# Performance work log

Measured on AMD Instinct MI355X. Metric: run time of the kernel, lower is better.

The kernel has to match this reference:

```python
import jax, jax.numpy as jnp
import numpy as np

N_NODES = 200000
N_GRAPHS = 64
K_SLOTS = 16
LATENT = 128
HID = 128  # hidden_dim // 2


def setup_inputs() -> dict:
    key = jax.random.key(0)
    ks = jax.random.split(key, 8)
    z = jax.random.normal(ks[0], (N_GRAPHS, K_SLOTS, LATENT), dtype=jnp.float32)
    s = jax.random.uniform(ks[1], (N_NODES, K_SLOTS), dtype=jnp.float32)
    batch = jnp.sort(jax.random.randint(ks[2], (N_NODES,), 0, N_GRAPHS))
    sc1 = 1.0 / np.sqrt(LATENT)
    sc2 = 1.0 / np.sqrt(HID)
    W1 = jax.random.normal(ks[3], (LATENT, HID), dtype=jnp.float32) * sc1
    b1 = jnp.zeros((HID,), dtype=jnp.float32)
    W2 = jax.random.normal(ks[4], (HID, HID), dtype=jnp.float32) * sc2
    b2 = jnp.zeros((HID,), dtype=jnp.float32)
    Wp = jax.random.normal(ks[5], (HID, 2), dtype=jnp.float32) * sc2
    bp = jnp.zeros((2,), dtype=jnp.float32)
    Wv = jax.random.normal(ks[6], (HID, 2), dtype=jnp.float32) * sc2
    bv = jnp.zeros((2,), dtype=jnp.float32)
    return {"z": z, "s": s, "batch": batch, "W1": W1, "b1": b1,
            "W2": W2, "b2": b2, "Wp": Wp, "bp": bp, "Wv": Wv, "bv": bv}


def reference(z, s, batch, W1, b1, W2, b2, Wp, bp, Wv, bv):
    # gather per-node latent set: [N, K, D]
    z_expanded = z[batch]
    # weighted sum over K slots -> [N, D]
    node_feat = jnp.einsum('nk,nkd->nd', s, z_expanded)
    # shared MLP: Linear-ReLU-Linear-ReLU
    h = jax.nn.relu(node_feat @ W1 + b1)
    h = jax.nn.relu(h @ W2 + b2)
    # heads
    pos_recon = jnp.tanh(h @ Wp + bp)
    vel_recon = h @ Wv + bv
    return jnp.concatenate([pos_recon, vel_recon], axis=-1)
```

## Files before the change

kernel.cpp:

```cpp
#include <hip/hip_runtime.h>

typedef _Float16 half4 __attribute__((ext_vector_type(4)));
typedef _Float16 half8 __attribute__((ext_vector_type(8)));
typedef float    f32x4 __attribute__((ext_vector_type(4)));

#define MFMA16(a,b,c) __builtin_amdgcn_mfma_f32_16x16x16f16((a),(b),(c),0,0,0)

static constexpr int N_NODES  = 200000;
static constexpr int N_GRAPHS = 64;
static constexpr int SGPG     = 128;
static constexpr int TOTAL_SG = N_GRAPHS * SGPG;

static constexpr size_t WS_ZWT    = 0;
static constexpr size_t WS_W2T    = 262144;
static constexpr size_t WS_WHT    = 294912;
static constexpr size_t WS_GSTART = 299008;


__global__ __launch_bounds__(256) void gnn_prep(
    const int* __restrict__ batch,
    const float* __restrict__ z,
    const float* __restrict__ W1,
    const float* __restrict__ W2,
    const float* __restrict__ Wp,
    const float* __restrict__ Wv,
    int* __restrict__ gstart,
    _Float16* __restrict__ zwt,
    _Float16* __restrict__ w2t,
    _Float16* __restrict__ wht)
{
    const int b = blockIdx.x, t = threadIdx.x;
    if (b < 782) {
        const int i = b * 256 + t;
        if (i < N_NODES) {
            const int bi   = batch[i];
            const int prev = (i == 0) ? -1 : batch[i - 1];
            if (bi != prev)
                for (int g = prev + 1; g <= bi; ++g) gstart[g] = i;
            if (i == N_NODES - 1)
                for (int g = bi + 1; g <= N_GRAPHS; ++g) gstart[g] = N_NODES;
        }
    } else if (b < 846) {
        const int e = (b - 782) * 256 + t;
        const int n = e >> 7, kk = e & 127;
        w2t[e] = (_Float16)W2[kk * 128 + n];
    } else if (b < 854) {
        const int e = (b - 846) * 256 + t;
        const int j = e >> 7, d = e & 127;
        float v = 0.f;
        if (j < 2)      v = Wp[d * 2 + j];
        else if (j < 4) v = Wv[d * 2 + (j - 2)];
        wht[e] = (_Float16)v;
    } else {
        const int p = (b - 854) * 2 + (t >> 7);
        const int g = p >> 4, k = p & 15, d = t & 127;
        const float* zr = z + (g * 16 + k) * 128;
        float a0 = 0.f, a1 = 0.f, a2 = 0.f, a3 = 0.f;
#pragma unroll 8
        for (int c = 0; c < 128; c += 4) {
            a0 += zr[c    ] * W1[(c    ) * 128 + d];
            a1 += zr[c + 1] * W1[(c + 1) * 128 + d];
            a2 += zr[c + 2] * W1[(c + 2) * 128 + d];
            a3 += zr[c + 3] * W1[(c + 3) * 128 + d];
        }
        zwt[(g * 128 + d) * 16 + k] = (_Float16)((a0 + a1) + (a2 + a3));
    }
}

__device__ inline float fast_tanh(float x) {
    x = fminf(fmaxf(x, -15.f), 15.f);
    const float e = __expf(2.f * x);
    return (e - 1.f) / (e + 1.f);
}

__global__ __launch_bounds__(256, 4) void gnn_main(
    const float* __restrict__ s,
    const float* __restrict__ b1,
    const float* __restrict__ b2,
    const float* __restrict__ bp,
    const float* __restrict__ bv,
    const _Float16* __restrict__ zwt,
    const _Float16* __restrict__ w2t,
    const _Float16* __restrict__ wht,
    const int* __restrict__ gstart,
    float* __restrict__ out)
{
    __shared__ char lds[37888];
    half8* a2l = (half8*)lds;
    half4* a3l = (half4*)(lds + 32768);
    float* b1l = (float*)(lds + 36864);
    float* b2l = (float*)(lds + 37376);

    const int tid  = threadIdx.x;
    const int lane = tid & 63;
    const int n16  = lane & 15;
    const int quad = lane >> 4;

#pragma unroll
    for (int r = 0; r < 8; ++r) {
        const int e  = r * 256 + tid;
        const int mo = e >> 8, tp = (e >> 6) & 3, ll = e & 63;
        const int nn = ll & 15, qq = ll >> 4;
        const _Float16* srcp = w2t + (mo * 16 + nn) * 128 + tp * 32 + qq * 4;
        half8 v;
        *(half4*)&v     = *(const half4*)srcp;
        *((half4*)&v+1) = *(const half4*)(srcp + 16);
        a2l[e] = v;
    }
    {
        const int e = tid;
#pragma unroll
        for (int r = 0; r < 2; ++r) {
            const int ee = r * 256 + e;
            const int tt = ee >> 6, ll = ee & 63;
            const int nn = ll & 15, qq = ll >> 4;
            a3l[ee] = *(const half4*)(wht + nn * 128 + tt * 16 + qq * 4);
        }
        if (tid < 128)      b1l[tid] = b1[tid];
        else                b2l[tid - 128] = b2[tid - 128];
    }
    __syncthreads();

    const float bp0 = bp[0], bp1 = bp[1], bv0 = bv[0], bv1 = bv[1];
    f32x4 c3init = {0.f, 0.f, 0.f, 0.f};
    if (quad == 0) { c3init[0] = bp0; c3init[1] = bp1; c3init[2] = bv0; c3init[3] = bv1; }

    const int wid = blockIdx.x * 4 + (tid >> 6);
    const int nw  = gridDim.x * 4;

    for (int sgi = wid; sgi < TOTAL_SG; sgi += nw) {
        const int g    = sgi >> 7;
        const int idx  = sgi & 127;
        const int gs   = gstart[g];
        const int ge   = gstart[g + 1];
        const int base = gs + idx * 32;
        if (base >= ge) continue;

        const int nodeA = base + n16;
        const int nodeB = base + 16 + n16;
        const bool vA = nodeA < ge;
        const bool vB = nodeB < ge;

        half4 bsA = {(_Float16)0.f, (_Float16)0.f, (_Float16)0.f, (_Float16)0.f};
        half4 bsB = bsA;
        if (vA) {
            const f32x4 sv = *(const f32x4*)(s + nodeA * 16 + quad * 4);
            bsA[0] = (_Float16)sv[0]; bsA[1] = (_Float16)sv[1];
            bsA[2] = (_Float16)sv[2]; bsA[3] = (_Float16)sv[3];
        }
        if (vB) {
            const f32x4 sv = *(const f32x4*)(s + nodeB * 16 + quad * 4);
            bsB[0] = (_Float16)sv[0]; bsB[1] = (_Float16)sv[1];
            bsB[2] = (_Float16)sv[2]; bsB[3] = (_Float16)sv[3];
        }

        const _Float16* zg = zwt + g * 2048;
        half4 h1a[8], h1b[8];
#pragma unroll
        for (int mt = 0; mt < 8; ++mt) {
            const half4 a1 = *(const half4*)(zg + (mt * 16 + n16) * 16 + quad * 4);
            const f32x4 cb = *(const f32x4*)(b1l + mt * 16 + quad * 4);
            const f32x4 accA = MFMA16(a1, bsA, cb);
            const f32x4 accB = MFMA16(a1, bsB, cb);
#pragma unroll
            for (int i = 0; i < 4; ++i) {
                h1a[mt][i] = (_Float16)fmaxf(accA[i], 0.f);
                h1b[mt][i] = (_Float16)fmaxf(accB[i], 0.f);
            }
        }

        f32x4 acc3a = c3init, acc3b = c3init;
#pragma unroll
        for (int mo = 0; mo < 8; ++mo) {
            const f32x4 cb = *(const f32x4*)(b2l + mo * 16 + quad * 4);
            f32x4 a2a = cb, a2b = cb;
#pragma unroll
            for (int tp = 0; tp < 4; ++tp) {
                const half8 w = a2l[(mo * 4 + tp) * 64 + lane];
                const half4 wlo = {w[0], w[1], w[2], w[3]};
                const half4 whi = {w[4], w[5], w[6], w[7]};
                a2a = MFMA16(wlo, h1a[tp * 2], a2a);
                a2a = MFMA16(whi, h1a[tp * 2 + 1], a2a);
                a2b = MFMA16(wlo, h1b[tp * 2], a2b);
                a2b = MFMA16(whi, h1b[tp * 2 + 1], a2b);
            }
            half4 h2a, h2b;
#pragma unroll
            for (int i = 0; i < 4; ++i) {
                h2a[i] = (_Float16)fmaxf(a2a[i], 0.f);
                h2b[i] = (_Float16)fmaxf(a2b[i], 0.f);
            }
            const half4 w3 = a3l[mo * 64 + lane];
            acc3a = MFMA16(w3, h2a, acc3a);
            acc3b = MFMA16(w3, h2b, acc3b);
        }

        if (quad == 0) {
            if (vA) {
                f32x4 o;
                o[0] = fast_tanh(acc3a[0]); o[1] = fast_tanh(acc3a[1]);
                o[2] = acc3a[2];            o[3] = acc3a[3];
                *(f32x4*)(out + nodeA * 4) = o;
            }
            if (vB) {
                f32x4 o;
                o[0] = fast_tanh(acc3b[0]); o[1] = fast_tanh(acc3b[1]);
                o[2] = acc3b[2];            o[3] = acc3b[3];
                *(f32x4*)(out + nodeB * 4) = o;
            }
        }
    }
}

extern "C" void kernel_launch(void* const* d_in, const int* in_sizes, int n_in,
                              void* d_out, int out_size, void* d_ws, size_t ws_size,
                              hipStream_t stream)
{
    const float* z     = (const float*)d_in[0];
    const float* s     = (const float*)d_in[1];
    const int*   batch = (const int*)d_in[2];
    const float* W1    = (const float*)d_in[3];
    const float* b1    = (const float*)d_in[4];
    const float* W2    = (const float*)d_in[5];
    const float* b2    = (const float*)d_in[6];
    const float* Wp    = (const float*)d_in[7];
    const float* bp    = (const float*)d_in[8];
    const float* Wv    = (const float*)d_in[9];
    const float* bv    = (const float*)d_in[10];
    float* out = (float*)d_out;

    char* w = (char*)d_ws;
    _Float16* zwt = (_Float16*)(w + WS_ZWT);
    _Float16* w2t = (_Float16*)(w + WS_W2T);
    _Float16* wht = (_Float16*)(w + WS_WHT);
    int* gstart   = (int*)(w + WS_GSTART);

    hipLaunchKernelGGL(gnn_prep, dim3(1366), dim3(256), 0, stream,
                       batch, z, W1, W2, Wp, Wv, gstart, zwt, w2t, wht);
    hipLaunchKernelGGL(gnn_main, dim3(1024), dim3(256), 0, stream,
                       s, b1, b2, bp, bv, zwt, w2t, wht, gstart, out);
}
```

Baseline: 113.7 us.

## Process fixed 64-node windows per wave, handling graph boundaries with masked MFMAs

Drops the gstart boundary computation from the prep kernel. The main kernel now walks contiguous 64-node windows, reads batch directly, and uses masked per-graph MFMA accumulation when a window spans several graphs. Each wave now handles four 16-node tiles instead of two, so every W2 fragment read from LDS is reused across more MFMAs, and conversions use packed cvt_pkrtz. The cost is higher register pressure, which is why launch bounds drop to 3 waves per SIMD and the grid shrinks. The window indexing assumes N_NODES is a multiple of 64.

```diff
diff --git a/kernel.cpp b/kernel.cpp
--- a/kernel.cpp
+++ b/kernel.cpp
@@ -1,5 +1,7 @@
 #include <hip/hip_runtime.h>
 
+typedef _Float16 half2 __attribute__((ext_vector_type(2)));
+typedef __fp16   fp16x2 __attribute__((ext_vector_type(2)));
 typedef _Float16 half4 __attribute__((ext_vector_type(4)));
 typedef _Float16 half8 __attribute__((ext_vector_type(8)));
 typedef float    f32x4 __attribute__((ext_vector_type(4)));
@@ -7,52 +9,37 @@
 #define MFMA16(a,b,c) __builtin_amdgcn_mfma_f32_16x16x16f16((a),(b),(c),0,0,0)
 
 static constexpr int N_NODES  = 200000;
-static constexpr int N_GRAPHS = 64;
-static constexpr int SGPG     = 128;
-static constexpr int TOTAL_SG = N_GRAPHS * SGPG;
-
-static constexpr size_t WS_ZWT    = 0;
-static constexpr size_t WS_W2T    = 262144;
-static constexpr size_t WS_WHT    = 294912;
-static constexpr size_t WS_GSTART = 299008;
+static constexpr int N_WIN    = N_NODES / 64;
+
+static constexpr size_t WS_ZWT = 0;
+static constexpr size_t WS_W2T = 262144;
+static constexpr size_t WS_WHT = 294912;
 
 
 __global__ __launch_bounds__(256) void gnn_prep(
-    const int* __restrict__ batch,
     const float* __restrict__ z,
     const float* __restrict__ W1,
     const float* __restrict__ W2,
     const float* __restrict__ Wp,
     const float* __restrict__ Wv,
-    int* __restrict__ gstart,
     _Float16* __restrict__ zwt,
     _Float16* __restrict__ w2t,
     _Float16* __restrict__ wht)
 {
     const int b = blockIdx.x, t = threadIdx.x;
-    if (b < 782) {
-        const int i = b * 256 + t;
-        if (i < N_NODES) {
-            const int bi   = batch[i];
-            const int prev = (i == 0) ? -1 : batch[i - 1];
-            if (bi != prev)
-                for (int g = prev + 1; g <= bi; ++g) gstart[g] = i;
-            if (i == N_NODES - 1)
-                for (int g = bi + 1; g <= N_GRAPHS; ++g) gstart[g] = N_NODES;
-        }
-    } else if (b < 846) {
-        const int e = (b - 782) * 256 + t;
+    if (b < 64) {
+        const int e = b * 256 + t;
         const int n = e >> 7, kk = e & 127;
         w2t[e] = (_Float16)W2[kk * 128 + n];
-    } else if (b < 854) {
-        const int e = (b - 846) * 256 + t;
+    } else if (b < 72) {
+        const int e = (b - 64) * 256 + t;
         const int j = e >> 7, d = e & 127;
         float v = 0.f;
         if (j < 2)      v = Wp[d * 2 + j];
         else if (j < 4) v = Wv[d * 2 + (j - 2)];
         wht[e] = (_Float16)v;
     } else {
-        const int p = (b - 854) * 2 + (t >> 7);
+        const int p = (b - 72) * 2 + (t >> 7);
         const int g = p >> 4, k = p & 15, d = t & 127;
         const float* zr = z + (g * 16 + k) * 128;
         float a0 = 0.f, a1 = 0.f, a2 = 0.f, a3 = 0.f;
@@ -73,8 +60,23 @@
     return (e - 1.f) / (e + 1.f);
 }
 
-__global__ __launch_bounds__(256, 4) void gnn_main(
+__device__ inline half4 cvt4(const f32x4 v) {
+    half4 r;
+    *(half2*)&r       = __builtin_bit_cast(half2, __builtin_amdgcn_cvt_pkrtz(v[0], v[1]));
+    *((half2*)&r + 1) = __builtin_bit_cast(half2, __builtin_amdgcn_cvt_pkrtz(v[2], v[3]));
+    return r;
+}
+
+__device__ inline half4 relu_cvt4(const f32x4 v) {
+    half4 r;
+    *(half2*)&r       = __builtin_bit_cast(half2, __builtin_amdgcn_cvt_pkrtz(fmaxf(v[0], 0.f), fmaxf(v[1], 0.f)));
+    *((half2*)&r + 1) = __builtin_bit_cast(half2, __builtin_amdgcn_cvt_pkrtz(fmaxf(v[2], 0.f), fmaxf(v[3], 0.f)));
+    return r;
+}
+
+__global__ __launch_bounds__(256, 3) void gnn_main(
     const float* __restrict__ s,
+    const int* __restrict__ batch,
     const float* __restrict__ b1,
     const float* __restrict__ b2,
     const float* __restrict__ bp,
@@ -82,7 +84,6 @@
     const _Float16* __restrict__ zwt,
     const _Float16* __restrict__ w2t,
     const _Float16* __restrict__ wht,
-    const int* __restrict__ gstart,
     float* __restrict__ out)
 {
     __shared__ char lds[37888];
@@ -103,110 +104,114 @@
         const int nn = ll & 15, qq = ll >> 4;
         const _Float16* srcp = w2t + (mo * 16 + nn) * 128 + tp * 32 + qq * 4;
         half8 v;
-        *(half4*)&v     = *(const half4*)srcp;
-        *((half4*)&v+1) = *(const half4*)(srcp + 16);
+        *(half4*)&v       = *(const half4*)srcp;
+        *((half4*)&v + 1) = *(const half4*)(srcp + 16);
         a2l[e] = v;
     }
-    {
-        const int e = tid;
-#pragma unroll
-        for (int r = 0; r < 2; ++r) {
-            const int ee = r * 256 + e;
-            const int tt = ee >> 6, ll = ee & 63;
-            const int nn = ll & 15, qq = ll >> 4;
-            a3l[ee] = *(const half4*)(wht + nn * 128 + tt * 16 + qq * 4);
-        }
-        if (tid < 128)      b1l[tid] = b1[tid];
-        else                b2l[tid - 128] = b2[tid - 128];
-    }
+#pragma unroll
+    for (int r = 0; r < 2; ++r) {
+        const int ee = r * 256 + tid;
+        const int tt = ee >> 6, ll = ee & 63;
+        const int nn = ll & 15, qq = ll >> 4;
+        a3l[ee] = *(const half4*)(wht + nn * 128 + tt * 16 + qq * 4);
+    }
+    if (tid < 128)      b1l[tid] = b1[tid];
+    else                b2l[tid - 128] = b2[tid - 128];
     __syncthreads();
 
-    const float bp0 = bp[0], bp1 = bp[1], bv0 = bv[0], bv1 = bv[1];
     f32x4 c3init = {0.f, 0.f, 0.f, 0.f};
-    if (quad == 0) { c3init[0] = bp0; c3init[1] = bp1; c3init[2] = bv0; c3init[3] = bv1; }
+    if (quad == 0) { c3init[0] = bp[0]; c3init[1] = bp[1]; c3init[2] = bv[0]; c3init[3] = bv[1]; }
 
     const int wid = blockIdx.x * 4 + (tid >> 6);
     const int nw  = gridDim.x * 4;
 
-    for (int sgi = wid; sgi < TOTAL_SG; sgi += nw) {
-        const int g    = sgi >> 7;
-        const int idx  = sgi & 127;
-        const int gs   = gstart[g];
-        const int ge   = gstart[g + 1];
-        const int base = gs + idx * 32;
-        if (base >= ge) continue;
-
-        const int nodeA = base + n16;
-        const int nodeB = base + 16 + n16;
-        const bool vA = nodeA < ge;
-        const bool vB = nodeB < ge;
-
-        half4 bsA = {(_Float16)0.f, (_Float16)0.f, (_Float16)0.f, (_Float16)0.f};
-        half4 bsB = bsA;
-        if (vA) {
-            const f32x4 sv = *(const f32x4*)(s + nodeA * 16 + quad * 4);
-            bsA[0] = (_Float16)sv[0]; bsA[1] = (_Float16)sv[1];
-            bsA[2] = (_Float16)sv[2]; bsA[3] = (_Float16)sv[3];
-        }
-        if (vB) {
-            const f32x4 sv = *(const f32x4*)(s + nodeB * 16 + quad * 4);
-            bsB[0] = (_Float16)sv[0]; bsB[1] = (_Float16)sv[1];
-            bsB[2] = (_Float16)sv[2]; bsB[3] = (_Float16)sv[3];
-        }
-
-        const _Float16* zg = zwt + g * 2048;
-        half4 h1a[8], h1b[8];
-#pragma unroll
-        for (int mt = 0; mt < 8; ++mt) {
-            const half4 a1 = *(const half4*)(zg + (mt * 16 + n16) * 16 + quad * 4);
-            const f32x4 cb = *(const f32x4*)(b1l + mt * 16 + quad * 4);
-            const f32x4 accA = MFMA16(a1, bsA, cb);
-            const f32x4 accB = MFMA16(a1, bsB, cb);
-#pragma unroll
-            for (int i = 0; i < 4; ++i) {
-                h1a[mt][i] = (_Float16)fmaxf(accA[i], 0.f);
-                h1b[mt][i] = (_Float16)fmaxf(accB[i], 0.f);
-            }
-        }
-
-        f32x4 acc3a = c3init, acc3b = c3init;
+    for (int w = wid; w < N_WIN; w += nw) {
+        const int base = w * 64;
+
+        f32x4 sv[4];
+#pragma unroll
+        for (int j = 0; j < 4; ++j)
+            sv[j] = *(const f32x4*)(s + (base + j * 16 + n16) * 16 + quad * 4);
+        const int gLo = batch[base];
+        const int gHi = batch[base + 63];
+
+        half4 bs[4];
+#pragma unroll
+        for (int j = 0; j < 4; ++j) bs[j] = cvt4(sv[j]);
+
+        half4 h1[4][8];
+        if (gLo == gHi) {
+            const _Float16* zg = zwt + gLo * 2048;
+#pragma unroll
+            for (int mt = 0; mt < 8; ++mt) {
+                const half4 a1 = *(const half4*)(zg + (mt * 16 + n16) * 16 + quad * 4);
+                const f32x4 cb = *(const f32x4*)(b1l + mt * 16 + quad * 4);
+#pragma unroll
+                for (int j = 0; j < 4; ++j)
+                    h1[j][mt] = relu_cvt4(MFMA16(a1, bs[j], cb));
+            }
+        } else {
+            int bg[4];
+#pragma unroll
+            for (int j = 0; j < 4; ++j) bg[j] = batch[base + j * 16 + n16];
+            const half4 z4 = {(_Float16)0.f, (_Float16)0.f, (_Float16)0.f, (_Float16)0.f};
+#pragma unroll
+            for (int mt = 0; mt < 8; ++mt) {
+                const f32x4 cb = *(const f32x4*)(b1l + mt * 16 + quad * 4);
+                f32x4 acc[4];
+#pragma unroll
+                for (int j = 0; j < 4; ++j) acc[j] = cb;
+                for (int g = gLo; g <= gHi; ++g) {
+                    const half4 a1 = *(const half4*)(zwt + (g * 128 + mt * 16 + n16) * 16 + quad * 4);
+#pragma unroll
+                    for (int j = 0; j < 4; ++j) {
+                        const half4 bm = (bg[j] == g) ? bs[j] : z4;
+                        acc[j] = MFMA16(a1, bm, acc[j]);
+                    }
+                }
+#pragma unroll
+                for (int j = 0; j < 4; ++j) h1[j][mt] = relu_cvt4(acc[j]);
+            }
+        }
+
+        f32x4 acc3[4];
+#pragma unroll
+        for (int j = 0; j < 4; ++j) acc3[j] = c3init;
 #pragma unroll
         for (int mo = 0; mo < 8; ++mo) {
             const f32x4 cb = *(const f32x4*)(b2l + mo * 16 + quad * 4);
-            f32x4 a2a = cb, a2b = cb;
+            f32x4 acc2[4];
+#pragma unroll
+            for (int j = 0; j < 4; ++j) acc2[j] = cb;
 #pragma unroll
             for (int tp = 0; tp < 4; ++tp) {
-                const half8 w = a2l[(mo * 4 + tp) * 64 + lane];
-                const half4 wlo = {w[0], w[1], w[2], w[3]};
-                const half4 whi = {w[4], w[5], w[6], w[7]};
-                a2a = MFMA16(wlo, h1a[tp * 2], a2a);
-                a2a = MFMA16(whi, h1a[tp * 2 + 1], a2a);
-                a2b = MFMA16(wlo, h1b[tp * 2], a2b);
-                a2b = MFMA16(whi, h1b[tp * 2 + 1], a2b);
-            }
-            half4 h2a, h2b;
-#pragma unroll
-            for (int i = 0; i < 4; ++i) {
-                h2a[i] = (_Float16)fmaxf(a2a[i], 0.f);
-                h2b[i] = (_Float16)fmaxf(a2b[i], 0.f);
+                const half8 ww = a2l[(mo * 4 + tp) * 64 + lane];
+                const half4 wlo = {ww[0], ww[1], ww[2], ww[3]};
+                const half4 whi = {ww[4], ww[5], ww[6], ww[7]};
+#pragma unroll
+                for (int j = 0; j < 4; ++j) {
+                    acc2[j] = MFMA16(wlo, h1[j][tp * 2], acc2[j]);
+                    acc2[j] = MFMA16(whi, h1[j][tp * 2 + 1], acc2[j]);
+                }
             }
             const half4 w3 = a3l[mo * 64 + lane];
-            acc3a = MFMA16(w3, h2a, acc3a);
-            acc3b = MFMA16(w3, h2b, acc3b);
+#pragma unroll
+            for (int j = 0; j < 4; ++j) {
+                const half4 h2 = relu_cvt4(acc2[j]);
+                acc3[j] = MFMA16(w3, h2, acc3[j]);
+            }
         }
 
         if (quad == 0) {
-            if (vA) {
+#pragma unroll
+            for (int j = 0; j < 4; ++j) {
+                const int node = base + j * 16 + n16;
                 f32x4 o;
-                o[0] = fast_tanh(acc3a[0]); o[1] = fast_tanh(acc3a[1]);
-                o[2] = acc3a[2];            o[3] = acc3a[3];
-                *(f32x4*)(out + nodeA * 4) = o;
-            }
-            if (vB) {
-                f32x4 o;
-                o[0] = fast_tanh(acc3b[0]); o[1] = fast_tanh(acc3b[1]);
-                o[2] = acc3b[2];            o[3] = acc3b[3];
-                *(f32x4*)(out + nodeB * 4) = o;
+                o[0] = fast_tanh(acc3[j][0]);
+                o[1] = fast_tanh(acc3[j][1]);
+                o[2] = acc3[j][2];
+                o[3] = acc3[j][3];
+                *(f32x4*)(out + node * 4) = o;
             }
         }
     }
@@ -233,10 +238,9 @@
     _Float16* zwt = (_Float16*)(w + WS_ZWT);
     _Float16* w2t = (_Float16*)(w + WS_W2T);
     _Float16* wht = (_Float16*)(w + WS_WHT);
-    int* gstart   = (int*)(w + WS_GSTART);
-
-    hipLaunchKernelGGL(gnn_prep, dim3(1366), dim3(256), 0, stream,
-                       batch, z, W1, W2, Wp, Wv, gstart, zwt, w2t, wht);
-    hipLaunchKernelGGL(gnn_main, dim3(1024), dim3(256), 0, stream,
-                       s, b1, b2, bp, bv, zwt, w2t, wht, gstart, out);
-}
+
+    hipLaunchKernelGGL(gnn_prep, dim3(584), dim3(256), 0, stream,
+                       z, W1, W2, Wp, Wv, zwt, w2t, wht);
+    hipLaunchKernelGGL(gnn_main, dim3(768), dim3(256), 0, stream,
+                       s, batch, b1, b2, bp, bv, zwt, w2t, wht, out);
+}
```

Result: slower. 143.4 us (+26.1%).
